# Optimization experiments

Hardware: AMD Instinct MI355X
Metric: run time of the kernel (lower is better)

The kernel has to match this reference:

```python
import jax, jax.numpy as jnp
import numpy as np
import math

N = 512
H = 512
L = 16384
R_MIN, R_MAX, MAX_PHASE = 0.0, 1.0, 6.283


def setup_inputs() -> dict:
    key = jax.random.key(0)
    ks = jax.random.split(key, 8)
    u1 = jax.random.uniform(ks[0], (N,))
    u2 = jax.random.uniform(ks[1], (N,))
    nu_log = jnp.log(-0.5 * jnp.log(u1 * (R_MAX ** 2 - R_MIN ** 2) + R_MIN ** 2))
    theta_log = jnp.log(u2 * MAX_PHASE)
    B_re = jax.random.normal(ks[2], (N, H)) / math.sqrt(2 * H)
    B_im = jax.random.normal(ks[3], (N, H)) / math.sqrt(2 * H)
    C_re = jax.random.normal(ks[4], (H, N)) / math.sqrt(N)
    C_im = jax.random.normal(ks[5], (H, N)) / math.sqrt(N)
    D = jax.random.normal(ks[6], (H,))
    diag_lambda = jnp.exp(-jnp.exp(nu_log) + 1j * jnp.exp(theta_log))
    gamma_log = jnp.log(jnp.sqrt(1.0 - jnp.abs(diag_lambda) ** 2))
    x = jax.random.normal(ks[7], (L, H), dtype=jnp.float32)
    # state is Lambda's multiplier in the original code; ones => standard LRU
    state_re = jnp.ones((N,), dtype=jnp.float32)
    state_im = jnp.zeros((N,), dtype=jnp.float32)
    return {"x": x, "state_re": state_re, "state_im": state_im,
            "nu_log": nu_log, "theta_log": theta_log, "gamma_log": gamma_log,
            "B_re": B_re, "B_im": B_im, "C_re": C_re, "C_im": C_im, "D": D}


def _binop(ei, ej):
    a_i, bu_i = ei
    a_j, bu_j = ej
    return (a_j * a_i, a_j * bu_i + bu_j)


def reference(x, state_re, state_im, nu_log, theta_log, gamma_log,
              B_re, B_im, C_re, C_im, D):
    Lambda = jnp.exp(-jnp.exp(nu_log) + 1j * jnp.exp(theta_log))  # (N,) c64
    # NOTE: original uses exp(i*gamma_log) (a phase), faithful here
    exp_gamma = jnp.exp(1j * gamma_log.astype(jnp.complex64))      # (N,)
    B = (B_re + 1j * B_im) * exp_gamma[:, None]                    # (N,H)
    C = C_re + 1j * C_im                                           # (H,N)
    state = state_re + 1j * state_im                               # (N,)
    a0 = Lambda * state                                            # (N,)
    a_elems = jnp.broadcast_to(a0, (x.shape[0], a0.shape[0]))      # (L,N)
    xc = x.astype(jnp.complex64)                                   # (L,H)
    Bu = xc @ B.T                                                  # (L,N)
    _, inner_states = jax.lax.associative_scan(_binop, (a_elems, Bu))
    y = jnp.real(inner_states @ C.T) + D[None, :] * x              # (L,H)
    return y
```

## Files before the change

kernel.cpp:

```cpp
#include <hip/hip_runtime.h>
#include <hip/hip_bf16.h>
#include <cstdint>

#define L_SEQ 16384
#define NST   512
#define HDIM  512
#define CH    512
#define CT    32

typedef __attribute__((ext_vector_type(8))) short short8;
typedef __attribute__((ext_vector_type(4))) float f32x4;

static __device__ __forceinline__ ushort f2bf(float f) {
  union { float f; unsigned int u; } v; v.f = f;
  unsigned int r = v.u + 0x7fffu + ((v.u >> 16) & 1u);
  return (ushort)(r >> 16);
}
static __device__ __forceinline__ float bf2f(ushort u) {
  union { unsigned int u; float f; } v; v.u = ((unsigned int)u) << 16;
  return v.f;
}

static __device__ __forceinline__ void mfma_16x16x32_bf16(f32x4& d, short8 a, short8 b) {
  asm("v_mfma_f32_16x16x32_bf16 %0, %1, %2, %0" : "+v"(d) : "v"(a), "v"(b));
}

static __device__ __forceinline__ void gload_lds16(const ushort* g, ushort* l) {
  __builtin_amdgcn_global_load_lds((__attribute__((address_space(1))) void*)(g),
                                   (__attribute__((address_space(3))) void*)(l),
                                   16, 0, 0);
}


__global__ __launch_bounds__(256) void setup_all(
    const float* __restrict__ st_re, const float* __restrict__ st_im,
    const float* __restrict__ nu_log, const float* __restrict__ theta_log,
    const float* __restrict__ gamma_log,
    const float* __restrict__ B_re, const float* __restrict__ B_im,
    const float* __restrict__ C_re, const float* __restrict__ C_im,
    const float* __restrict__ X,
    float2* __restrict__ lam, float2* __restrict__ lamT,
    ushort* __restrict__ W1, ushort* __restrict__ W2,
    ushort* __restrict__ xb)
{
  int bid = blockIdx.x, tid = threadIdx.x;
  if (bid < 4096) {
    size_t i = ((size_t)bid * 256 + tid) * 8;
#pragma unroll
    for (int j = 0; j < 8; j += 4) {
      float4 v = *(const float4*)(X + i + j);
      ushort4 o;
      o.x = f2bf(v.x); o.y = f2bf(v.y); o.z = f2bf(v.z); o.w = f2bf(v.w);
      *(ushort4*)(xb + i + j) = o;
    }
  } else if (bid < 5120) {
    int idx = (bid - 4096) * 256 + tid;
    int n = idx >> 9, h = idx & 511;
    float g = gamma_log[n];
    float sg, cg; sincosf(g, &sg, &cg);
    float br = B_re[idx], bi = B_im[idx];
    W1[(size_t)(2 * n) * 512 + h]     = f2bf(br * cg - bi * sg);
    W1[(size_t)(2 * n + 1) * 512 + h] = f2bf(br * sg + bi * cg);
  } else if (bid < 6144) {
    int idx = (bid - 5120) * 256 + tid;
    int hh = idx >> 9, n = idx & 511;
    W2[(size_t)hh * 1024 + 2 * n]     = f2bf(C_re[idx]);
    W2[(size_t)hh * 1024 + 2 * n + 1] = f2bf(-C_im[idx]);
  } else {
    int n = (bid - 6144) * 256 + tid;
    float nu  = expf(nu_log[n]);
    float th  = expf(theta_log[n]);
    float mag = expf(-nu);
    float sth, cth; sincosf(th, &sth, &cth);
    float lr = mag * cth, li = mag * sth;
    float sr = st_re[n], si = st_im[n];
    float ar = lr * sr - li * si;
    float ai = lr * si + li * sr;
    lam[n] = make_float2(ar, ai);
    float pr = ar, pi = ai;
#pragma unroll
    for (int i = 0; i < 5; ++i) {
      float nr = pr * pr - pi * pi;
      float ni = 2.f * pr * pi;
      pr = nr; pi = ni;
    }
    lamT[n] = make_float2(pr, pi);
  }
}

template <int BM, int BN, int WMW, int WNW, int EPI>
__global__ __launch_bounds__(WMW * WNW * 64, 2)
void gemm_p(const ushort* __restrict__ A, const ushort* __restrict__ Bm,
            ushort* __restrict__ Cb, float* __restrict__ Cf,
            const float* __restrict__ Dv, const ushort* __restrict__ Xb,
            const float2* __restrict__ lam, float2* __restrict__ carry,
            int M, int Ncols, int K)
{
  constexpr int THREADS = WMW * WNW * 64;
  constexpr int FM = BM / (WMW * 16);
  constexpr int FN = BN / (WNW * 16);
  constexpr int SLOT = (BM + BN) * 32;
  constexpr int GR = (BM + BN) * 4;
  constexpr int LPT = GR / THREADS;
  static_assert(LPT == 4, "vmcnt immediates assume 4 loads/thread/tile");
  __shared__ __align__(16) ushort lds[4 * SLOT];

  const int t = threadIdx.x, lane = t & 63, w = t >> 6;
  const int wr = w / WNW, wc = w % WNW;
  const int m0 = blockIdx.x * BM, n0 = blockIdx.y * BN;
  const int rr = lane & 15, kk = (lane >> 4) * 8;
  const int swzu = ((rr >> 1) & 3) << 3;
  const int NK = K / 32;

  f32x4 acc[FM][FN];
#pragma unroll
  for (int i = 0; i < FM; ++i)
#pragma unroll
    for (int j = 0; j < FN; ++j) { f32x4 z = {0.f, 0.f, 0.f, 0.f}; acc[i][j] = z; }

  auto stage = [&](int kt) {
    int k0 = kt * 32;
    ushort* base = lds + (kt & 3) * SLOT;
#pragma unroll
    for (int j = 0; j < LPT; ++j) {
      int d = j * THREADS + t;
      const ushort* g;
      if (d < BM * 4) {
        int row = d >> 2;
        int sl  = (d & 3) ^ ((row >> 1) & 3);
        g = A + (size_t)(m0 + row) * K + k0 + sl * 8;
      } else {
        int dd = d - BM * 4;
        int row = dd >> 2;
        int sl  = (dd & 3) ^ ((row >> 1) & 3);
        g = Bm + (size_t)(n0 + row) * K + k0 + sl * 8;
      }
      gload_lds16(g, base + d * 8);
    }
  };

  stage(0); stage(1); stage(2);
  asm volatile("s_waitcnt vmcnt(8)" ::: "memory");
  asm volatile("s_barrier" ::: "memory");

  for (int kt = 0; kt < NK; ++kt) {
    const ushort* As = lds + (kt & 3) * SLOT;
    const ushort* Bs = As + BM * 32;
    short8 af[FM], bb[FN];
#pragma unroll
    for (int mi = 0; mi < FM; ++mi)
      af[mi] = *(const short8*)(As + (wr * FM * 16 + mi * 16 + rr) * 32 + (kk ^ swzu));
#pragma unroll
    for (int ni = 0; ni < FN; ++ni)
      bb[ni] = *(const short8*)(Bs + (wc * FN * 16 + ni * 16 + rr) * 32 + (kk ^ swzu));
    if (kt + 3 < NK) stage(kt + 3);
    asm volatile("s_waitcnt lgkmcnt(0)" ::: "memory");
    __builtin_amdgcn_sched_barrier(0);
    __builtin_amdgcn_s_setprio(1);
#pragma unroll
    for (int mi = 0; mi < FM; ++mi)
#pragma unroll
      for (int ni = 0; ni < FN; ++ni)
        mfma_16x16x32_bf16(acc[mi][ni], af[mi], bb[ni]);
    __builtin_amdgcn_s_setprio(0);
    __builtin_amdgcn_sched_barrier(0);
    if (kt < NK - 3)       asm volatile("s_waitcnt vmcnt(8)" ::: "memory");
    else if (kt == NK - 3) asm volatile("s_waitcnt vmcnt(4)" ::: "memory");
    else                   asm volatile("s_waitcnt vmcnt(0)" ::: "memory");
    asm volatile("s_barrier" ::: "memory");
  }

  const int crow = (lane >> 4) * 4, ccol = lane & 15;
#pragma unroll
  for (int mi = 0; mi < FM; ++mi) {
#pragma unroll
    for (int ni = 0; ni < FN; ++ni) {
      int col = n0 + wc * FN * 16 + ni * 16 + ccol;
#pragma unroll
      for (int r = 0; r < 4; ++r) {
        int row = m0 + wr * FM * 16 + mi * 16 + crow + r;
        float v = acc[mi][ni][r];
        size_t idx = (size_t)row * Ncols + col;
        if (EPI == 0) Cb[idx] = f2bf(v);
        else          Cf[idx] = v + Dv[col] * bf2f(Xb[idx]);
      }
    }
  }

  if (EPI == 0) {
    asm volatile("s_waitcnt vmcnt(0)" ::: "memory");
    __syncthreads();
#pragma unroll
    for (int task = 0; task < 2; ++task) {
      int c  = (t >> 7) + task * 4;
      int ch = t & 127;
      float2 a = lam[(n0 >> 1) + ch];
      float cr = 0.f, ci = 0.f;
      const ushort* p = Cb + (size_t)(m0 + c * 32) * Ncols + n0 + 2 * ch;
#pragma unroll 8
      for (int r = 0; r < 32; ++r) {
        ushort2 v = *(const ushort2*)(p + (size_t)r * Ncols);
        float br = bf2f(v.x), bi = bf2f(v.y);
        float nr = a.x * cr - a.y * ci + br;
        float ni = a.x * ci + a.y * cr + bi;
        cr = nr; ci = ni;
      }
      carry[(size_t)((n0 >> 1) + ch) * CH + (m0 >> 5) + c] = make_float2(cr, ci);
    }
  }
}

__global__ __launch_bounds__(CH) void scanC(const float2* __restrict__ carry,
                                            const float2* __restrict__ lamT,
                                            float2* __restrict__ prefix)
{
  int n = blockIdx.x;
  int c = threadIdx.x;
  __shared__ float2 buf[CH];
  float2 aT = lamT[n];
  float2 v = carry[(size_t)n * CH + c];
  buf[c] = v;
  __syncthreads();
  float mr = aT.x, mi = aT.y;
#pragma unroll
  for (int s = 1; s < CH; s <<= 1) {
    float2 o = make_float2(0.f, 0.f);
    if (c >= s) o = buf[c - s];
    __syncthreads();
    v.x += mr * o.x - mi * o.y;
    v.y += mr * o.y + mi * o.x;
    buf[c] = v;
    __syncthreads();
    float nmr = mr * mr - mi * mi;
    float nmi = 2.f * mr * mi;
    mr = nmr; mi = nmi;
  }
  float2 p = (c == 0) ? make_float2(0.f, 0.f) : buf[c - 1];
  prefix[(size_t)n * CH + c] = p;
}

__global__ __launch_bounds__(256) void scanB(ushort* __restrict__ Bu,
                                             const float2* __restrict__ lam,
                                             const float2* __restrict__ prefix)
{
  int q = threadIdx.x;
  int c = blockIdx.x;
  float2 a0 = lam[2 * q], a1 = lam[2 * q + 1];
  float2 g0 = prefix[(size_t)(2 * q) * CH + c];
  float2 g1 = prefix[(size_t)(2 * q + 1) * CH + c];
  float hr0 = g0.x, hi0 = g0.y, hr1 = g1.x, hi1 = g1.y;
  ushort* base = Bu + (size_t)c * CT * 1024 + 4 * q;
#pragma unroll 4
  for (int tt = 0; tt < CT; ++tt) {
    ushort4 v = *(const ushort4*)(base + tt * 1024);
    float nr0 = a0.x * hr0 - a0.y * hi0 + bf2f(v.x);
    float ni0 = a0.x * hi0 + a0.y * hr0 + bf2f(v.y);
    hr0 = nr0; hi0 = ni0;
    float nr1 = a1.x * hr1 - a1.y * hi1 + bf2f(v.z);
    float ni1 = a1.x * hi1 + a1.y * hr1 + bf2f(v.w);
    hr1 = nr1; hi1 = ni1;
    ushort4 o;
    o.x = f2bf(hr0); o.y = f2bf(hi0);
    o.z = f2bf(hr1); o.w = f2bf(hi1);
    *(ushort4*)(base + tt * 1024) = o;
  }
}

extern "C" void kernel_launch(void* const* d_in, const int* in_sizes, int n_in,
                              void* d_out, int out_size, void* d_ws, size_t ws_size,
                              hipStream_t stream)
{
  const float* x         = (const float*)d_in[0];
  const float* state_re  = (const float*)d_in[1];
  const float* state_im  = (const float*)d_in[2];
  const float* nu_log    = (const float*)d_in[3];
  const float* theta_log = (const float*)d_in[4];
  const float* gamma_log = (const float*)d_in[5];
  const float* B_re      = (const float*)d_in[6];
  const float* B_im      = (const float*)d_in[7];
  const float* C_re      = (const float*)d_in[8];
  const float* C_im      = (const float*)d_in[9];
  const float* Dv        = (const float*)d_in[10];
  float* y = (float*)d_out;

  char* ws = (char*)d_ws;
  size_t off = 0;
  float2* lam    = (float2*)(ws + off); off += 4096;
  float2* lamT   = (float2*)(ws + off); off += 4096;
  float2* carry  = (float2*)(ws + off); off += (size_t)CH * NST * sizeof(float2);
  float2* prefix = (float2*)(ws + off); off += (size_t)CH * NST * sizeof(float2);
  ushort* W1 = (ushort*)(ws + off); off += (size_t)2 * NST * HDIM * sizeof(ushort);
  ushort* W2 = (ushort*)(ws + off); off += (size_t)HDIM * 2 * NST * sizeof(ushort);
  ushort* xb = (ushort*)(ws + off); off += (size_t)L_SEQ * HDIM * sizeof(ushort);
  ushort* Bu = (ushort*)(ws + off); off += (size_t)L_SEQ * 2 * NST * sizeof(ushort);

  setup_all<<<6146, 256, 0, stream>>>(state_re, state_im, nu_log, theta_log,
                                      gamma_log, B_re, B_im, C_re, C_im, x,
                                      lam, lamT, W1, W2, xb);

  gemm_p<256, 256, 2, 4, 0><<<dim3(L_SEQ / 256, (2 * NST) / 256), 512, 0, stream>>>(
      xb, W1, Bu, nullptr, nullptr, nullptr, lam, carry, L_SEQ, 2 * NST, HDIM);

  scanC<<<NST, CH, 0, stream>>>(carry, lamT, prefix);
  scanB<<<CH, 256, 0, stream>>>(Bu, lam, prefix);

  gemm_p<128, 128, 2, 2, 1><<<dim3(L_SEQ / 128, HDIM / 128), 256, 0, stream>>>(
      Bu, W2, nullptr, y, Dv, xb, nullptr, nullptr, L_SEQ, HDIM, 2 * NST);
}
```

Baseline: 84.99 us.

## Fuse all stages into one persistent kernel with software grid barriers

```diff
diff --git a/kernel.cpp b/kernel.cpp
--- a/kernel.cpp
+++ b/kernel.cpp
@@ -7,6 +7,8 @@
 #define HDIM  512
 #define CH    512
 #define CT    32
+#define NBLK  256
+#define NTHR  512
 
 typedef __attribute__((ext_vector_type(8))) short short8;
 typedef __attribute__((ext_vector_type(4))) float f32x4;
@@ -31,83 +33,37 @@
                                    16, 0, 0);
 }
 
-
-__global__ __launch_bounds__(256) void setup_all(
-    const float* __restrict__ st_re, const float* __restrict__ st_im,
-    const float* __restrict__ nu_log, const float* __restrict__ theta_log,
-    const float* __restrict__ gamma_log,
-    const float* __restrict__ B_re, const float* __restrict__ B_im,
-    const float* __restrict__ C_re, const float* __restrict__ C_im,
-    const float* __restrict__ X,
-    float2* __restrict__ lam, float2* __restrict__ lamT,
-    ushort* __restrict__ W1, ushort* __restrict__ W2,
-    ushort* __restrict__ xb)
-{
-  int bid = blockIdx.x, tid = threadIdx.x;
-  if (bid < 4096) {
-    size_t i = ((size_t)bid * 256 + tid) * 8;
-#pragma unroll
-    for (int j = 0; j < 8; j += 4) {
-      float4 v = *(const float4*)(X + i + j);
-      ushort4 o;
-      o.x = f2bf(v.x); o.y = f2bf(v.y); o.z = f2bf(v.z); o.w = f2bf(v.w);
-      *(ushort4*)(xb + i + j) = o;
-    }
-  } else if (bid < 5120) {
-    int idx = (bid - 4096) * 256 + tid;
-    int n = idx >> 9, h = idx & 511;
-    float g = gamma_log[n];
-    float sg, cg; sincosf(g, &sg, &cg);
-    float br = B_re[idx], bi = B_im[idx];
-    W1[(size_t)(2 * n) * 512 + h]     = f2bf(br * cg - bi * sg);
-    W1[(size_t)(2 * n + 1) * 512 + h] = f2bf(br * sg + bi * cg);
-  } else if (bid < 6144) {
-    int idx = (bid - 5120) * 256 + tid;
-    int hh = idx >> 9, n = idx & 511;
-    W2[(size_t)hh * 1024 + 2 * n]     = f2bf(C_re[idx]);
-    W2[(size_t)hh * 1024 + 2 * n + 1] = f2bf(-C_im[idx]);
-  } else {
-    int n = (bid - 6144) * 256 + tid;
-    float nu  = expf(nu_log[n]);
-    float th  = expf(theta_log[n]);
-    float mag = expf(-nu);
-    float sth, cth; sincosf(th, &sth, &cth);
-    float lr = mag * cth, li = mag * sth;
-    float sr = st_re[n], si = st_im[n];
-    float ar = lr * sr - li * si;
-    float ai = lr * si + li * sr;
-    lam[n] = make_float2(ar, ai);
-    float pr = ar, pi = ai;
-#pragma unroll
-    for (int i = 0; i < 5; ++i) {
-      float nr = pr * pr - pi * pi;
-      float ni = 2.f * pr * pi;
-      pr = nr; pi = ni;
-    }
-    lamT[n] = make_float2(pr, pi);
-  }
+static __device__ __forceinline__ void gbar(unsigned* cnt, unsigned target) {
+  __syncthreads();
+  if (threadIdx.x == 0) {
+    __threadfence();
+    atomicAdd(cnt, 1u);
+    while (atomicAdd(cnt, 0u) < target)
+      __builtin_amdgcn_s_sleep(8);
+  }
+  __syncthreads();
+  __threadfence();
 }
 
 template <int BM, int BN, int WMW, int WNW, int EPI>
-__global__ __launch_bounds__(WMW * WNW * 64, 2)
-void gemm_p(const ushort* __restrict__ A, const ushort* __restrict__ Bm,
-            ushort* __restrict__ Cb, float* __restrict__ Cf,
-            const float* __restrict__ Dv, const ushort* __restrict__ Xb,
-            const float2* __restrict__ lam, float2* __restrict__ carry,
-            int M, int Ncols, int K)
+static __device__ __forceinline__ void gemm_phase(
+    ushort* smem,
+    const ushort* __restrict__ A, const ushort* __restrict__ Bm,
+    ushort* __restrict__ Cb, float* __restrict__ Cf,
+    const float* __restrict__ Dv, const ushort* __restrict__ Xb,
+    const float2* __restrict__ lam, float2* __restrict__ carry,
+    int m0, int n0, int Ncols, int K)
 {
   constexpr int THREADS = WMW * WNW * 64;
+  static_assert(THREADS == NTHR, "phase must use full block");
   constexpr int FM = BM / (WMW * 16);
   constexpr int FN = BN / (WNW * 16);
   constexpr int SLOT = (BM + BN) * 32;
-  constexpr int GR = (BM + BN) * 4;
-  constexpr int LPT = GR / THREADS;
-  static_assert(LPT == 4, "vmcnt immediates assume 4 loads/thread/tile");
-  __shared__ __align__(16) ushort lds[4 * SLOT];
+  constexpr int LPT  = (BM + BN) * 4 / THREADS;
+  static_assert(LPT == 3 || LPT == 4, "vmcnt immediates cover LPT 3/4");
 
   const int t = threadIdx.x, lane = t & 63, w = t >> 6;
   const int wr = w / WNW, wc = w % WNW;
-  const int m0 = blockIdx.x * BM, n0 = blockIdx.y * BN;
   const int rr = lane & 15, kk = (lane >> 4) * 8;
   const int swzu = ((rr >> 1) & 3) << 3;
   const int NK = K / 32;
@@ -120,7 +76,7 @@
 
   auto stage = [&](int kt) {
     int k0 = kt * 32;
-    ushort* base = lds + (kt & 3) * SLOT;
+    ushort* base = smem + (kt & 3) * SLOT;
 #pragma unroll
     for (int j = 0; j < LPT; ++j) {
       int d = j * THREADS + t;
@@ -140,11 +96,12 @@
   };
 
   stage(0); stage(1); stage(2);
-  asm volatile("s_waitcnt vmcnt(8)" ::: "memory");
+  if constexpr (LPT == 4) asm volatile("s_waitcnt vmcnt(8)" ::: "memory");
+  else                    asm volatile("s_waitcnt vmcnt(6)" ::: "memory");
   asm volatile("s_barrier" ::: "memory");
 
   for (int kt = 0; kt < NK; ++kt) {
-    const ushort* As = lds + (kt & 3) * SLOT;
+    const ushort* As = smem + (kt & 3) * SLOT;
     const ushort* Bs = As + BM * 32;
     short8 af[FM], bb[FN];
 #pragma unroll
@@ -164,9 +121,15 @@
         mfma_16x16x32_bf16(acc[mi][ni], af[mi], bb[ni]);
     __builtin_amdgcn_s_setprio(0);
     __builtin_amdgcn_sched_barrier(0);
-    if (kt < NK - 3)       asm volatile("s_waitcnt vmcnt(8)" ::: "memory");
-    else if (kt == NK - 3) asm volatile("s_waitcnt vmcnt(4)" ::: "memory");
-    else                   asm volatile("s_waitcnt vmcnt(0)" ::: "memory");
+    if constexpr (LPT == 4) {
+      if (kt < NK - 3)       asm volatile("s_waitcnt vmcnt(8)" ::: "memory");
+      else if (kt == NK - 3) asm volatile("s_waitcnt vmcnt(4)" ::: "memory");
+      else                   asm volatile("s_waitcnt vmcnt(0)" ::: "memory");
+    } else {
+      if (kt < NK - 3)       asm volatile("s_waitcnt vmcnt(6)" ::: "memory");
+      else if (kt == NK - 3) asm volatile("s_waitcnt vmcnt(3)" ::: "memory");
+      else                   asm volatile("s_waitcnt vmcnt(0)" ::: "memory");
+    }
     asm volatile("s_barrier" ::: "memory");
   }
 
@@ -181,13 +144,13 @@
         int row = m0 + wr * FM * 16 + mi * 16 + crow + r;
         float v = acc[mi][ni][r];
         size_t idx = (size_t)row * Ncols + col;
-        if (EPI == 0) Cb[idx] = f2bf(v);
-        else          Cf[idx] = v + Dv[col] * bf2f(Xb[idx]);
+        if constexpr (EPI == 0) Cb[idx] = f2bf(v);
+        else                    Cf[idx] = v + Dv[col] * bf2f(Xb[idx]);
       }
     }
   }
 
-  if (EPI == 0) {
+  if constexpr (EPI == 0) {
     asm volatile("s_waitcnt vmcnt(0)" ::: "memory");
     __syncthreads();
 #pragma unroll
@@ -210,60 +173,132 @@
   }
 }
 
-__global__ __launch_bounds__(CH) void scanC(const float2* __restrict__ carry,
-                                            const float2* __restrict__ lamT,
-                                            float2* __restrict__ prefix)
+__global__ __launch_bounds__(NTHR, 2) void mega(
+    const float* __restrict__ st_re, const float* __restrict__ st_im,
+    const float* __restrict__ nu_log, const float* __restrict__ theta_log,
+    const float* __restrict__ gamma_log,
+    const float* __restrict__ B_re, const float* __restrict__ B_im,
+    const float* __restrict__ C_re, const float* __restrict__ C_im,
+    const float* __restrict__ X, const float* __restrict__ Dv,
+    float* __restrict__ y, unsigned* __restrict__ bar,
+    float2* __restrict__ lam, float2* __restrict__ lamT,
+    float2* __restrict__ carry, float2* __restrict__ prefix,
+    ushort* __restrict__ W1, ushort* __restrict__ W2,
+    ushort* __restrict__ xb, ushort* __restrict__ Bu)
 {
-  int n = blockIdx.x;
-  int c = threadIdx.x;
-  __shared__ float2 buf[CH];
-  float2 aT = lamT[n];
-  float2 v = carry[(size_t)n * CH + c];
-  buf[c] = v;
-  __syncthreads();
-  float mr = aT.x, mi = aT.y;
-#pragma unroll
-  for (int s = 1; s < CH; s <<= 1) {
-    float2 o = make_float2(0.f, 0.f);
-    if (c >= s) o = buf[c - s];
-    __syncthreads();
-    v.x += mr * o.x - mi * o.y;
-    v.y += mr * o.y + mi * o.x;
-    buf[c] = v;
-    __syncthreads();
-    float nmr = mr * mr - mi * mi;
-    float nmi = 2.f * mr * mi;
-    mr = nmr; mi = nmi;
-  }
-  float2 p = (c == 0) ? make_float2(0.f, 0.f) : buf[c - 1];
-  prefix[(size_t)n * CH + c] = p;
-}
-
-__global__ __launch_bounds__(256) void scanB(ushort* __restrict__ Bu,
-                                             const float2* __restrict__ lam,
-                                             const float2* __restrict__ prefix)
-{
-  int q = threadIdx.x;
-  int c = blockIdx.x;
-  float2 a0 = lam[2 * q], a1 = lam[2 * q + 1];
-  float2 g0 = prefix[(size_t)(2 * q) * CH + c];
-  float2 g1 = prefix[(size_t)(2 * q + 1) * CH + c];
-  float hr0 = g0.x, hi0 = g0.y, hr1 = g1.x, hi1 = g1.y;
-  ushort* base = Bu + (size_t)c * CT * 1024 + 4 * q;
+  __shared__ __align__(16) ushort smem[65536];
+  const int bid = blockIdx.x, tid = threadIdx.x;
+  const int g = bid * NTHR + tid;
+
+  for (int idx = g; idx < (L_SEQ * HDIM) / 8; idx += NBLK * NTHR) {
+    size_t i = (size_t)idx * 8;
+#pragma unroll
+    for (int j = 0; j < 8; j += 4) {
+      float4 v = *(const float4*)(X + i + j);
+      ushort4 o;
+      o.x = f2bf(v.x); o.y = f2bf(v.y); o.z = f2bf(v.z); o.w = f2bf(v.w);
+      *(ushort4*)(xb + i + j) = o;
+    }
+  }
+  for (int idx = g; idx < NST * HDIM; idx += NBLK * NTHR) {
+    int n = idx >> 9, h = idx & 511;
+    float gm = gamma_log[n];
+    float sg, cg; sincosf(gm, &sg, &cg);
+    float br = B_re[idx], bi = B_im[idx];
+    W1[(size_t)(2 * n) * 512 + h]     = f2bf(br * cg - bi * sg);
+    W1[(size_t)(2 * n + 1) * 512 + h] = f2bf(br * sg + bi * cg);
+  }
+  for (int idx = g; idx < NST * HDIM; idx += NBLK * NTHR) {
+    int hh = idx >> 9, n = idx & 511;
+    W2[(size_t)hh * 1024 + 2 * n]     = f2bf(C_re[idx]);
+    W2[(size_t)hh * 1024 + 2 * n + 1] = f2bf(-C_im[idx]);
+  }
+  if (g < NST) {
+    int n = g;
+    float nu  = expf(nu_log[n]);
+    float th  = expf(theta_log[n]);
+    float mag = expf(-nu);
+    float sth, cth; sincosf(th, &sth, &cth);
+    float lr = mag * cth, li = mag * sth;
+    float sr = st_re[n], si = st_im[n];
+    float ar = lr * sr - li * si;
+    float ai = lr * si + li * sr;
+    lam[n] = make_float2(ar, ai);
+    float pr = ar, pi = ai;
+#pragma unroll
+    for (int i = 0; i < 5; ++i) {
+      float nr = pr * pr - pi * pi;
+      float ni = 2.f * pr * pi;
+      pr = nr; pi = ni;
+    }
+    lamT[n] = make_float2(pr, pi);
+  }
+  gbar(bar, NBLK);
+
+  gemm_phase<256, 256, 2, 4, 0>(smem, xb, W1, Bu, nullptr, nullptr, nullptr,
+                                lam, carry, (bid >> 2) * 256, (bid & 3) * 256,
+                                2 * NST, HDIM);
+  gbar(bar, 2 * NBLK);
+
+  {
+    float2* buf = reinterpret_cast<float2*>(smem);
+    for (int rep = 0; rep < 2; ++rep) {
+      __syncthreads();
+      int n = bid + rep * NBLK;
+      int c = tid;
+      float2 aT = lamT[n];
+      float2 v = carry[(size_t)n * CH + c];
+      buf[c] = v;
+      __syncthreads();
+      float mr = aT.x, mi = aT.y;
+#pragma unroll
+      for (int s = 1; s < CH; s <<= 1) {
+        float2 o = make_float2(0.f, 0.f);
+        if (c >= s) o = buf[c - s];
+        __syncthreads();
+        v.x += mr * o.x - mi * o.y;
+        v.y += mr * o.y + mi * o.x;
+        buf[c] = v;
+        __syncthreads();
+        float nmr = mr * mr - mi * mi;
+        float nmi = 2.f * mr * mi;
+        mr = nmr; mi = nmi;
+      }
+      float2 p = (c == 0) ? make_float2(0.f, 0.f) : buf[c - 1];
+      prefix[(size_t)n * CH + c] = p;
+    }
+  }
+  gbar(bar, 3 * NBLK);
+
+  {
+    int c = bid * 2 + (tid >> 8);
+    int q = tid & 255;
+    float2 a0 = lam[2 * q], a1 = lam[2 * q + 1];
+    float2 g0 = prefix[(size_t)(2 * q) * CH + c];
+    float2 g1 = prefix[(size_t)(2 * q + 1) * CH + c];
+    float hr0 = g0.x, hi0 = g0.y, hr1 = g1.x, hi1 = g1.y;
+    ushort* base = Bu + (size_t)c * CT * 1024 + 4 * q;
 #pragma unroll 4
-  for (int tt = 0; tt < CT; ++tt) {
-    ushort4 v = *(const ushort4*)(base + tt * 1024);
-    float nr0 = a0.x * hr0 - a0.y * hi0 + bf2f(v.x);
-    float ni0 = a0.x * hi0 + a0.y * hr0 + bf2f(v.y);
-    hr0 = nr0; hi0 = ni0;
-    float nr1 = a1.x * hr1 - a1.y * hi1 + bf2f(v.z);
-    float ni1 = a1.x * hi1 + a1.y * hr1 + bf2f(v.w);
-    hr1 = nr1; hi1 = ni1;
-    ushort4 o;
-    o.x = f2bf(hr0); o.y = f2bf(hi0);
-    o.z = f2bf(hr1); o.w = f2bf(hi1);
-    *(ushort4*)(base + tt * 1024) = o;
-  }
+    for (int tt = 0; tt < CT; ++tt) {
+      ushort4 v = *(const ushort4*)(base + tt * 1024);
+      float nr0 = a0.x * hr0 - a0.y * hi0 + bf2f(v.x);
+      float ni0 = a0.x * hi0 + a0.y * hr0 + bf2f(v.y);
+      hr0 = nr0; hi0 = ni0;
+      float nr1 = a1.x * hr1 - a1.y * hi1 + bf2f(v.z);
+      float ni1 = a1.x * hi1 + a1.y * hr1 + bf2f(v.w);
+      hr1 = nr1; hi1 = ni1;
+      ushort4 o;
+      o.x = f2bf(hr0); o.y = f2bf(hi0);
+      o.z = f2bf(hr1); o.w = f2bf(hi1);
+      *(ushort4*)(base + tt * 1024) = o;
+    }
+  }
+  gbar(bar, 4 * NBLK);
+
+  gemm_phase<128, 256, 2, 4, 1>(smem, Bu, W2, nullptr, y, Dv, xb,
+                                nullptr, nullptr,
+                                (bid >> 1) * 128, (bid & 1) * 256,
+                                HDIM, 2 * NST);
 }
 
 extern "C" void kernel_launch(void* const* d_in, const int* in_sizes, int n_in,
@@ -285,6 +320,7 @@
 
   char* ws = (char*)d_ws;
   size_t off = 0;
+  unsigned* bar  = (unsigned*)(ws + off); off += 128;
   float2* lam    = (float2*)(ws + off); off += 4096;
   float2* lamT   = (float2*)(ws + off); off += 4096;
   float2* carry  = (float2*)(ws + off); off += (size_t)CH * NST * sizeof(float2);
@@ -294,16 +330,9 @@
   ushort* xb = (ushort*)(ws + off); off += (size_t)L_SEQ * HDIM * sizeof(ushort);
   ushort* Bu = (ushort*)(ws + off); off += (size_t)L_SEQ * 2 * NST * sizeof(ushort);
 
-  setup_all<<<6146, 256, 0, stream>>>(state_re, state_im, nu_log, theta_log,
-                                      gamma_log, B_re, B_im, C_re, C_im, x,
-                                      lam, lamT, W1, W2, xb);
-
-  gemm_p<256, 256, 2, 4, 0><<<dim3(L_SEQ / 256, (2 * NST) / 256), 512, 0, stream>>>(
-      xb, W1, Bu, nullptr, nullptr, nullptr, lam, carry, L_SEQ, 2 * NST, HDIM);
-
-  scanC<<<NST, CH, 0, stream>>>(carry, lamT, prefix);
-  scanB<<<CH, 256, 0, stream>>>(Bu, lam, prefix);
-
-  gemm_p<128, 128, 2, 2, 1><<<dim3(L_SEQ / 128, HDIM / 128), 256, 0, stream>>>(
-      Bu, W2, nullptr, y, Dv, xb, nullptr, nullptr, L_SEQ, HDIM, 2 * NST);
-}
+  hipMemsetAsync(bar, 0, 128, stream);
+  mega<<<NBLK, NTHR, 0, stream>>>(state_re, state_im, nu_log, theta_log,
+                                  gamma_log, B_re, B_im, C_re, C_im, x, Dv,
+                                  y, bar, lam, lamT, carry, prefix,
+                                  W1, W2, xb, Bu);
+}
```

After: 281.3 us. 3.31x slower.
